# Optimization experiments

Measured on AMD Instinct MI355X. Metric: run time of the kernel, lower is better.

## Reference

```python
import jax, jax.numpy as jnp
import numpy as np

B, C, H, W = 4, 192, 56, 56


def setup_inputs() -> dict:
    key = jax.random.key(0)
    k1, k2, k3 = jax.random.split(key, 3)
    x = jax.random.normal(k1, (B, C, H, W), dtype=jnp.float32)
    conv_w = jax.random.normal(k2, (C, 2 * C), dtype=jnp.float32) * (1.0 / np.sqrt(2 * C))
    conv_b = jax.random.normal(k3, (C,), dtype=jnp.float32) * 0.01
    bn_gamma = jnp.ones((C,), dtype=jnp.float32)
    bn_beta = jnp.zeros((C,), dtype=jnp.float32)
    bn_mean = jnp.zeros((C,), dtype=jnp.float32)
    bn_var = jnp.ones((C,), dtype=jnp.float32)
    return {"x": x, "conv_w": conv_w, "conv_b": conv_b, "bn_gamma": bn_gamma,
            "bn_beta": bn_beta, "bn_mean": bn_mean, "bn_var": bn_var, "K": 4}


def reference(x, conv_w, conv_b, bn_gamma, bn_beta, bn_mean, bn_var, K):
    b, c, h, w = x.shape
    shifts_h = list(range(0, h, K))          # rolls along H
    shifts_w = list(range(K, w, K))          # rolls along W
    n = len(shifts_h) + len(shifts_w)
    scale = n ** (-0.5)
    # (B, n, C, H, W): all circularly shifted copies (static shift set)
    rolled = jnp.stack([jnp.roll(x, i, axis=2) for i in shifts_h] +
                       [jnp.roll(x, j, axis=3) for j in shifts_w], axis=1)
    # scores: tanh(scale * x * x_rolled), summed over channels -> (B, n, 1, H, W)
    scores = jnp.tanh(rolled * x[:, None] * scale).sum(axis=2, keepdims=True)
    weights = jax.nn.softmax(scores, axis=1)
    out = (rolled * weights).sum(axis=1)     # (B, C, H, W)
    cat = jnp.concatenate([x, out], axis=1)  # (B, 2C, H, W)
    # 1x1 conv as GEMM over channels
    y = jnp.einsum('bchw,oc->bohw', cat, conv_w) + conv_b[None, :, None, None]
    # BatchNorm2d in eval mode (running stats)
    eps = 1e-5
    inv = bn_gamma / jnp.sqrt(bn_var + eps)
    y = (y - bn_mean[None, :, None, None]) * inv[None, :, None, None] + bn_beta[None, :, None, None]
    return jax.nn.gelu(y, approximate=False)
```

## Files before the change

### kernel.cpp

```cpp
#include <hip/hip_runtime.h>
#include <hip/hip_bf16.h>
#include <math.h>

#define BB 4
#define CC 192
#define HH 56
#define WW 56
#define HWW 3136

typedef __attribute__((ext_vector_type(8))) short short8;
typedef __attribute__((ext_vector_type(4))) float f32x4;

__device__ __forceinline__ unsigned short f2b(float f) {
    __hip_bfloat16 h = __float2bfloat16(f);
    return __builtin_bit_cast(unsigned short, h);
}
__device__ __forceinline__ float b2f(unsigned short u) {
    unsigned int x = ((unsigned int)u) << 16;
    return __builtin_bit_cast(float, x);
}
__device__ __forceinline__ void fma4(float4& a, float w, const float4& x) {
    a.x += w * x.x; a.y += w * x.y; a.z += w * x.z; a.w += w * x.w;
}

__global__ __launch_bounds__(256) void k_pre(const float* __restrict__ x,
                                             const float* __restrict__ cw,
                                             float* __restrict__ xt,
                                             unsigned short* __restrict__ cwh,
                                             unsigned short* __restrict__ cwl) {
    int tid = threadIdx.x, bid = blockIdx.x;
    if (bid < 2352) {
        __shared__ float tile[32][33];
        int b = bid / 588, rem = bid % 588;
        int by = rem / 98, bx = rem % 98;
        int tx = tid & 31, ty = tid >> 5;
        int p0 = bx * 32, c0 = by * 32;
#pragma unroll
        for (int i = 0; i < 4; i++) {
            int c = c0 + ty + 8 * i;
            tile[ty + 8 * i][tx] = x[(b * CC + c) * HWW + p0 + tx];
        }
        __syncthreads();
#pragma unroll
        for (int i = 0; i < 4; i++) {
            int p = p0 + ty + 8 * i;
            xt[(size_t)(b * HWW + p) * CC + c0 + tx] = tile[tx][ty + 8 * i];
        }
    } else {
        int i = (bid - 2352) * 256 + tid;
        if (i < 384 * 192) {
            int n = i / 192, k = i % 192;
            float v = (n < 192) ? cw[n * 384 + k] : cw[(n - 192) * 384 + 192 + k];
            unsigned short hi = f2b(v);
            cwh[i] = hi;
            cwl[i] = f2b(v - b2f(hi));
        }
    }
}

__global__ __launch_bounds__(256) void k_mid(const float* __restrict__ xt,
                                             const unsigned short* __restrict__ cwh,
                                             const unsigned short* __restrict__ cwl,
                                             float* __restrict__ sp,
                                             float* __restrict__ u,
                                             float* __restrict__ z) {
    __shared__ __align__(16) char smem[36864];
    int tid = threadIdx.x, bid = blockIdx.x;

    if (bid < 1792) {
        float* Xs = (float*)smem;
        const float K2 = 0.38490017945975050f;
        bool isH = bid < 896;
        int lid = isH ? bid : bid - 896;
        int half = lid & 1;
        int rp = (lid >> 1) & 1;
        int cb2 = lid >> 2;
        int b = cb2 / 56, l0 = cb2 % 56;
        int r0 = rp * 2;

        const float* src = xt + (size_t)(b * HWW) * CC + half * 96;
        for (int idx = tid; idx < 28 * 24; idx += 256) {
            int t2 = idx / 24, cq = idx % 24;
            int pi = (r0 + t2 / 14) + 4 * (t2 % 14);
            int pix = isH ? (pi * WW + l0) : (l0 * WW + pi);
            float4 v = *(const float4*)(src + (size_t)pix * CC + cq * 4);
            *(float4*)&Xs[t2 * 100 + cq * 4] = v;
        }
        __syncthreads();

        int perCls = isH ? 105 : 91;
        if (tid < 2 * perCls) {
            int cls = tid / perCls, p = tid % perCls;
            int a, bb;
            if (isH) {
                a = (int)((sqrtf((float)(8 * p + 1)) - 1.0f) * 0.5f);
                bb = p - (a * (a + 1)) / 2;
            } else {
                int ap = (int)((sqrtf((float)(8 * p + 1)) - 1.0f) * 0.5f);
                bb = p - (ap * (ap + 1)) / 2;
                a = ap + 1;
            }
            const float* pA = &Xs[(cls * 14 + a) * 100];
            const float* pB = &Xs[(cls * 14 + bb) * 100];
            float s0 = 0.f, s1 = 0.f, s2 = 0.f, s3 = 0.f;
#pragma unroll
            for (int q = 0; q < 24; q++) {
                float4 av = *(const float4*)(pA + q * 4);
                float4 bv = *(const float4*)(pB + q * 4);
                s0 += __builtin_amdgcn_rcpf(__expf(av.x * bv.x * K2) + 1.0f);
                s1 += __builtin_amdgcn_rcpf(__expf(av.y * bv.y * K2) + 1.0f);
                s2 += __builtin_amdgcn_rcpf(__expf(av.z * bv.z * K2) + 1.0f);
                s3 += __builtin_amdgcn_rcpf(__expf(av.w * bv.w * K2) + 1.0f);
            }
            float s = 96.0f - 2.0f * (s0 + s1 + s2 + s3);
            int r = r0 + cls;
            size_t base = (size_t)(half * BB + b) * HWW;
            if (isH) {
                int i1 = a - bb;
                int h1 = r + 4 * a, h2 = r + 4 * bb;
                sp[(base + h1 * WW + l0) * 32 + i1] = s;
                if (a != bb) sp[(base + h2 * WW + l0) * 32 + (14 - i1)] = s;
            } else {
                int d = a - bb;
                int w1 = r + 4 * a, w2 = r + 4 * bb;
                sp[(base + l0 * WW + w1) * 32 + 14 + (d - 1)] = s;
                sp[(base + l0 * WW + w2) * 32 + 14 + (13 - d)] = s;
            }
        }
        return;
    }

    {
        unsigned short* Ah = (unsigned short*)smem;
        unsigned short* Al = Ah + 64 * 72;
        unsigned short* Bh = Ah + 2 * 64 * 72;
        unsigned short* Bl = Ah + 3 * 64 * 72;
        float* Ds = (float*)smem;
        int vb = bid - 1792;
        int bm = (vb % 196) * 64, bn = (vb / 196) * 64;
        int lane = tid & 63, wv = tid >> 6;

        f32x4 acc[4] = {{0,0,0,0},{0,0,0,0},{0,0,0,0},{0,0,0,0}};

        for (int kc = 0; kc < 3; kc++) {
#pragma unroll
            for (int r2 = 0; r2 < 2; r2++) {
                int idx = tid + r2 * 256;
                int m = idx >> 3, kq = idx & 7;
                const float* s = xt + (size_t)(bm + m) * CC + kc * 64 + kq * 8;
                float4 v0 = *(const float4*)s;
                float4 v1 = *(const float4*)(s + 4);
                float vv[8] = {v0.x, v0.y, v0.z, v0.w, v1.x, v1.y, v1.z, v1.w};
                unsigned short hi[8], lo[8];
#pragma unroll
                for (int e = 0; e < 8; e++) {
                    hi[e] = f2b(vv[e]);
                    lo[e] = f2b(vv[e] - b2f(hi[e]));
                }
                *(short8*)&Ah[m * 72 + kq * 8] = *(short8*)hi;
                *(short8*)&Al[m * 72 + kq * 8] = *(short8*)lo;
                size_t bo = (size_t)(bn + m) * 192 + kc * 64 + kq * 8;
                *(short8*)&Bh[m * 72 + kq * 8] = *(const short8*)(cwh + bo);
                *(short8*)&Bl[m * 72 + kq * 8] = *(const short8*)(cwl + bo);
            }
            __syncthreads();
            int n0 = wv * 16;
            int k8 = lane >> 4;
            int col = lane & 15;
#pragma unroll
            for (int ks = 0; ks < 64; ks += 32) {
                int koff = ks + k8 * 8;
                short8 bfh = *(const short8*)&Bh[(n0 + col) * 72 + koff];
                short8 bfl = *(const short8*)&Bl[(n0 + col) * 72 + koff];
#pragma unroll
                for (int fm = 0; fm < 4; fm++) {
                    short8 afh = *(const short8*)&Ah[(fm * 16 + col) * 72 + koff];
                    short8 afl = *(const short8*)&Al[(fm * 16 + col) * 72 + koff];
                    acc[fm] = __builtin_amdgcn_mfma_f32_16x16x32_bf16(afh, bfh, acc[fm], 0, 0, 0);
                    acc[fm] = __builtin_amdgcn_mfma_f32_16x16x32_bf16(afl, bfh, acc[fm], 0, 0, 0);
                    acc[fm] = __builtin_amdgcn_mfma_f32_16x16x32_bf16(afh, bfl, acc[fm], 0, 0, 0);
                }
            }
            __syncthreads();
        }
        {
            int col = lane & 15, rowq = lane >> 4;
#pragma unroll
            for (int fm = 0; fm < 4; fm++)
#pragma unroll
                for (int rg = 0; rg < 4; rg++)
                    Ds[(fm * 16 + rowq * 4 + rg) * 68 + wv * 16 + col] = acc[fm][rg];
        }
        __syncthreads();
        {
            int c4 = tid & 15, m0 = tid >> 4;
            int cg = bn + c4 * 4;
            float* dst = (cg < 192) ? u : z;
            int cc = (cg < 192) ? cg : cg - 192;
#pragma unroll
            for (int p = 0; p < 4; p++) {
                int m = m0 + p * 16;
                float4 v = *(float4*)&Ds[m * 68 + c4 * 4];
                *(float4*)&dst[(size_t)(bm + m) * CC + cc] = v;
            }
        }
    }
}

__global__ __launch_bounds__(192) void k_accH(const float* __restrict__ u,
                                              const float* __restrict__ z,
                                              const float* __restrict__ sp,
                                              float* __restrict__ yp) {
    __shared__ float Wt[14 * 56];
    int bid = blockIdx.x, tid = threadIdx.x;
    int b = bid / 56, l0 = bid % 56;

    if (tid < 56) {
        int pix = tid * WW + l0;
        const float4* p0 = (const float4*)&sp[((size_t)(0 * BB + b) * HWW + pix) * 32];
        const float4* p1 = (const float4*)&sp[((size_t)(1 * BB + b) * HWW + pix) * 32];
        float sc[28];
#pragma unroll
        for (int j = 0; j < 7; j++) {
            float4 a = p0[j], v = p1[j];
            sc[4 * j + 0] = a.x + v.x; sc[4 * j + 1] = a.y + v.y;
            sc[4 * j + 2] = a.z + v.z; sc[4 * j + 3] = a.w + v.w;
        }
        float mx = -1e30f;
#pragma unroll
        for (int s = 0; s < 27; s++) mx = fmaxf(mx, sc[s]);
        float sum = 0.f;
#pragma unroll
        for (int s = 0; s < 27; s++) { sc[s] = __expf(sc[s] - mx); sum += sc[s]; }
        float inv = __builtin_amdgcn_rcpf(sum);
#pragma unroll
        for (int i = 0; i < 14; i++) Wt[i * 56 + tid] = sc[i] * inv;
    }
    __syncthreads();
    {
        int r = tid & 3, q = tid >> 2;
        float4 in[14];
#pragma unroll
        for (int t = 0; t < 14; t++) {
            int pix = (r + 4 * t) * WW + l0;
            in[t] = *(const float4*)(z + (size_t)(b * HWW + pix) * CC + q * 4);
        }
        float4 acc[14];
#pragma unroll
        for (int a = 0; a < 14; a++) {
            int pix = (r + 4 * a) * WW + l0;
            acc[a] = *(const float4*)(u + (size_t)(b * HWW + pix) * CC + q * 4);
        }
#pragma unroll
        for (int i = 0; i < 14; i++)
#pragma unroll
            for (int a = 0; a < 14; a++)
                fma4(acc[a], Wt[i * 56 + (r + 4 * a)], in[(a - i + 14) % 14]);
#pragma unroll
        for (int a = 0; a < 14; a++) {
            int pix = (r + 4 * a) * WW + l0;
            *(float4*)(yp + (size_t)(b * HWW + pix) * CC + q * 4) = acc[a];
        }
    }
}

__global__ __launch_bounds__(192) void k_accW(const float* __restrict__ yp,
                                              const float* __restrict__ z,
                                              const float* __restrict__ sp,
                                              const float* __restrict__ cb,
                                              const float* __restrict__ gma,
                                              const float* __restrict__ bta,
                                              const float* __restrict__ mea,
                                              const float* __restrict__ var,
                                              float* __restrict__ y) {
    __shared__ float Wt[14 * 56];
    __shared__ float Ys[56 * 196];
    int bid = blockIdx.x, tid = threadIdx.x;
    int b = bid / 56, l0 = bid % 56;

    if (tid < 56) {
        int pix = l0 * WW + tid;
        const float4* p0 = (const float4*)&sp[((size_t)(0 * BB + b) * HWW + pix) * 32];
        const float4* p1 = (const float4*)&sp[((size_t)(1 * BB + b) * HWW + pix) * 32];
        float sc[28];
#pragma unroll
        for (int j = 0; j < 7; j++) {
            float4 a = p0[j], v = p1[j];
            sc[4 * j + 0] = a.x + v.x; sc[4 * j + 1] = a.y + v.y;
            sc[4 * j + 2] = a.z + v.z; sc[4 * j + 3] = a.w + v.w;
        }
        float mx = -1e30f;
#pragma unroll
        for (int s = 0; s < 27; s++) mx = fmaxf(mx, sc[s]);
        float sum = 0.f;
#pragma unroll
        for (int s = 0; s < 27; s++) { sc[s] = __expf(sc[s] - mx); sum += sc[s]; }
        float inv = __builtin_amdgcn_rcpf(sum);
#pragma unroll
        for (int j = 0; j < 13; j++) Wt[j * 56 + tid] = sc[14 + j] * inv;
    }
    __syncthreads();
    {
        int r = tid & 3, q = tid >> 2;
        float4 in[14];
#pragma unroll
        for (int t = 0; t < 14; t++) {
            int pix = l0 * WW + (r + 4 * t);
            in[t] = *(const float4*)(z + (size_t)(b * HWW + pix) * CC + q * 4);
        }
        float4 acc[14];
#pragma unroll
        for (int a = 0; a < 14; a++) {
            int pix = l0 * WW + (r + 4 * a);
            acc[a] = *(const float4*)(yp + (size_t)(b * HWW + pix) * CC + q * 4);
        }
#pragma unroll
        for (int j = 0; j < 13; j++)
#pragma unroll
            for (int a = 0; a < 14; a++)
                fma4(acc[a], Wt[j * 56 + (r + 4 * a)], in[(a - j - 1 + 14) % 14]);

        float4 bias4 = *(const float4*)&cb[q * 4];
        float4 g4 = *(const float4*)&gma[q * 4];
        float4 bt4 = *(const float4*)&bta[q * 4];
        float4 me4 = *(const float4*)&mea[q * 4];
        float4 va4 = *(const float4*)&var[q * 4];
        float inv0 = g4.x * rsqrtf(va4.x + 1e-5f);
        float inv1 = g4.y * rsqrtf(va4.y + 1e-5f);
        float inv2 = g4.z * rsqrtf(va4.z + 1e-5f);
        float inv3 = g4.w * rsqrtf(va4.w + 1e-5f);
#pragma unroll
        for (int a = 0; a < 14; a++) {
            int w = r + 4 * a;
            float4 t = acc[a];
            t.x = (t.x + bias4.x - me4.x) * inv0 + bt4.x;
            t.y = (t.y + bias4.y - me4.y) * inv1 + bt4.y;
            t.z = (t.z + bias4.z - me4.z) * inv2 + bt4.z;
            t.w = (t.w + bias4.w - me4.w) * inv3 + bt4.w;
            t.x = 0.5f * t.x * (1.0f + erff(t.x * 0.70710678118654752f));
            t.y = 0.5f * t.y * (1.0f + erff(t.y * 0.70710678118654752f));
            t.z = 0.5f * t.z * (1.0f + erff(t.z * 0.70710678118654752f));
            t.w = 0.5f * t.w * (1.0f + erff(t.w * 0.70710678118654752f));
            *(float4*)&Ys[w * 196 + q * 4] = t;
        }
    }
    __syncthreads();
    {
        int c = tid;
#pragma unroll
        for (int w4 = 0; w4 < 14; w4++) {
            float4 v;
            v.x = Ys[(w4 * 4 + 0) * 196 + c];
            v.y = Ys[(w4 * 4 + 1) * 196 + c];
            v.z = Ys[(w4 * 4 + 2) * 196 + c];
            v.w = Ys[(w4 * 4 + 3) * 196 + c];
            *(float4*)&y[(size_t)(b * CC + c) * HWW + l0 * WW + w4 * 4] = v;
        }
    }
}

extern "C" void kernel_launch(void* const* d_in, const int* in_sizes, int n_in,
                              void* d_out, int out_size, void* d_ws, size_t ws_size,
                              hipStream_t stream) {
    const float* x   = (const float*)d_in[0];
    const float* cw  = (const float*)d_in[1];
    const float* cb  = (const float*)d_in[2];
    const float* gma = (const float*)d_in[3];
    const float* bta = (const float*)d_in[4];
    const float* mea = (const float*)d_in[5];
    const float* var = (const float*)d_in[6];
    float* out = (float*)d_out;

    float* ws = (float*)d_ws;
    float*          xt  = ws;
    float*          sp  = ws + 2408448;
    float*          u   = ws + 3211264;
    float*          z   = ws + 5619712;
    float*          yp  = ws + 8028160;
    unsigned short* cwh = (unsigned short*)(ws + 10436608);
    unsigned short* cwl = (unsigned short*)(ws + 10473472);

    k_pre<<<2640, 256, 0, stream>>>(x, cw, xt, cwh, cwl);
    k_mid<<<2968, 256, 0, stream>>>(xt, cwh, cwl, sp, u, z);
    k_accH<<<224, 192, 0, stream>>>(u, z, sp, yp);
    k_accW<<<224, 192, 0, stream>>>(yp, z, sp, cb, gma, bta, mea, var, out);
}
```

Baseline: 127.9 us.

## Split softmax into its own kernel and fuse H/W accumulation with epilogue

Moves the per-pixel softmax over the 27 shift scores into a separate small kernel that writes normalized weights. The H-roll and W-roll accumulation passes are merged into one kernel tiled by (batch, residue r, 8-channel group, half of H). Each block stages a 14x56x8 slab of z in shared memory, so both shift directions read from LDS. This removes the yp intermediate round trip and gives 768 blocks instead of 224 for better occupancy. In exchange, each thread reloads 28 weights per pixel from global memory, and the output store writes one float per thread with a stride across channels.

```diff
diff --git a/kernel.cpp b/kernel.cpp
--- a/kernel.cpp
+++ b/kernel.cpp
@@ -18,9 +18,6 @@
 __device__ __forceinline__ float b2f(unsigned short u) {
     unsigned int x = ((unsigned int)u) << 16;
     return __builtin_bit_cast(float, x);
-}
-__device__ __forceinline__ void fma4(float4& a, float w, const float4& x) {
-    a.x += w * x.x; a.y += w * x.y; a.z += w * x.z; a.w += w * x.w;
 }
 
 __global__ __launch_bounds__(256) void k_pre(const float* __restrict__ x,
@@ -207,155 +204,117 @@
     }
 }
 
-__global__ __launch_bounds__(192) void k_accH(const float* __restrict__ u,
-                                              const float* __restrict__ z,
-                                              const float* __restrict__ sp,
-                                              float* __restrict__ yp) {
-    __shared__ float Wt[14 * 56];
-    int bid = blockIdx.x, tid = threadIdx.x;
-    int b = bid / 56, l0 = bid % 56;
-
-    if (tid < 56) {
-        int pix = tid * WW + l0;
-        const float4* p0 = (const float4*)&sp[((size_t)(0 * BB + b) * HWW + pix) * 32];
-        const float4* p1 = (const float4*)&sp[((size_t)(1 * BB + b) * HWW + pix) * 32];
-        float sc[28];
-#pragma unroll
-        for (int j = 0; j < 7; j++) {
-            float4 a = p0[j], v = p1[j];
-            sc[4 * j + 0] = a.x + v.x; sc[4 * j + 1] = a.y + v.y;
-            sc[4 * j + 2] = a.z + v.z; sc[4 * j + 3] = a.w + v.w;
-        }
-        float mx = -1e30f;
-#pragma unroll
-        for (int s = 0; s < 27; s++) mx = fmaxf(mx, sc[s]);
-        float sum = 0.f;
-#pragma unroll
-        for (int s = 0; s < 27; s++) { sc[s] = __expf(sc[s] - mx); sum += sc[s]; }
-        float inv = __builtin_amdgcn_rcpf(sum);
-#pragma unroll
-        for (int i = 0; i < 14; i++) Wt[i * 56 + tid] = sc[i] * inv;
+__global__ __launch_bounds__(256) void k_soft(const float* __restrict__ sp,
+                                              float* __restrict__ wn) {
+    int gp = blockIdx.x * 256 + threadIdx.x;
+    const float4* p0 = (const float4*)&sp[(size_t)gp * 32];
+    const float4* p1 = (const float4*)&sp[((size_t)(4 * HWW) + gp) * 32];
+    float sc[28];
+#pragma unroll
+    for (int j = 0; j < 7; j++) {
+        float4 a = p0[j], v = p1[j];
+        sc[4 * j + 0] = a.x + v.x; sc[4 * j + 1] = a.y + v.y;
+        sc[4 * j + 2] = a.z + v.z; sc[4 * j + 3] = a.w + v.w;
+    }
+    float mx = -1e30f;
+#pragma unroll
+    for (int s = 0; s < 27; s++) mx = fmaxf(mx, sc[s]);
+    float sum = 0.f;
+#pragma unroll
+    for (int s = 0; s < 27; s++) { sc[s] = __expf(sc[s] - mx); sum += sc[s]; }
+    float inv = __builtin_amdgcn_rcpf(sum);
+#pragma unroll
+    for (int s = 0; s < 27; s++) sc[s] *= inv;
+    sc[27] = 0.f;
+    float4* dst = (float4*)(wn + (size_t)gp * 28);
+#pragma unroll
+    for (int j = 0; j < 7; j++)
+        dst[j] = make_float4(sc[4 * j], sc[4 * j + 1], sc[4 * j + 2], sc[4 * j + 3]);
+}
+
+__global__ __launch_bounds__(448) void k_accHW(const float* __restrict__ u,
+                                               const float* __restrict__ z,
+                                               const float* __restrict__ wn,
+                                               const float* __restrict__ cb,
+                                               const float* __restrict__ gma,
+                                               const float* __restrict__ bta,
+                                               const float* __restrict__ mea,
+                                               const float* __restrict__ var,
+                                               float* __restrict__ y) {
+    __shared__ float Zs[14 * 56 * 8];
+    int tid = threadIdx.x, bid = blockIdx.x;
+    int th = bid & 1;
+    int t1 = bid >> 1;
+    int cc = t1 % 24;
+    int t2 = t1 / 24;
+    int r = t2 & 3;
+    int b = t2 >> 2;
+    int w = tid >> 3, c = tid & 7;
+    int cg = cc * 8 + c;
+
+#pragma unroll
+    for (int it = 0; it < 2; it++) {
+        int idx = tid + it * 448;
+        if (idx < 784) {
+            int t = idx / 56, ww = idx - t * 56;
+            const float* s = z + ((size_t)(b * HWW + (r + 4 * t) * WW + ww)) * CC + cc * 8;
+            float4 v0 = *(const float4*)s;
+            float4 v1 = *(const float4*)(s + 4);
+            float* d = &Zs[(t * 56 + ww) * 8];
+            *(float4*)d = v0;
+            *(float4*)(d + 4) = v1;
+        }
     }
     __syncthreads();
-    {
-        int r = tid & 3, q = tid >> 2;
-        float4 in[14];
-#pragma unroll
-        for (int t = 0; t < 14; t++) {
-            int pix = (r + 4 * t) * WW + l0;
-            in[t] = *(const float4*)(z + (size_t)(b * HWW + pix) * CC + q * 4);
-        }
-        float4 acc[14];
-#pragma unroll
-        for (int a = 0; a < 14; a++) {
-            int pix = (r + 4 * a) * WW + l0;
-            acc[a] = *(const float4*)(u + (size_t)(b * HWW + pix) * CC + q * 4);
-        }
+
+    float zc[14];
+#pragma unroll
+    for (int m = 0; m < 14; m++) {
+        int t0 = m + th * 7;
+        if (t0 >= 14) t0 -= 14;
+        zc[m] = Zs[(t0 * 56 + w) * 8 + c];
+    }
+
+    float bias = cb[cg];
+    float ginv = gma[cg] * rsqrtf(var[cg] + 1e-5f);
+    float bt = bta[cg];
+    float me = mea[cg];
+
+    int hbase = r + 4 * (th * 7);
+    float acc[7];
+#pragma unroll
+    for (int tt = 0; tt < 7; tt++) {
+        int pix = (hbase + 4 * tt) * WW + w;
+        acc[tt] = u[((size_t)(b * HWW + pix)) * CC + cg];
+    }
+
+#pragma unroll
+    for (int tt = 0; tt < 7; tt++) {
+        int t = th * 7 + tt;
+        int pix = (hbase + 4 * tt) * WW + w;
+        size_t gp = (size_t)b * HWW + pix;
+        const float4* wp = (const float4*)(wn + gp * 28);
+        float wt[28];
+        *(float4*)&wt[0]  = wp[0];
+        *(float4*)&wt[4]  = wp[1];
+        *(float4*)&wt[8]  = wp[2];
+        *(float4*)&wt[12] = wp[3];
+        *(float4*)&wt[16] = wp[4];
+        *(float4*)&wt[20] = wp[5];
+        *(float4*)&wt[24] = wp[6];
+        float a = acc[tt];
 #pragma unroll
         for (int i = 0; i < 14; i++)
-#pragma unroll
-            for (int a = 0; a < 14; a++)
-                fma4(acc[a], Wt[i * 56 + (r + 4 * a)], in[(a - i + 14) % 14]);
-#pragma unroll
-        for (int a = 0; a < 14; a++) {
-            int pix = (r + 4 * a) * WW + l0;
-            *(float4*)(yp + (size_t)(b * HWW + pix) * CC + q * 4) = acc[a];
-        }
-    }
-}
-
-__global__ __launch_bounds__(192) void k_accW(const float* __restrict__ yp,
-                                              const float* __restrict__ z,
-                                              const float* __restrict__ sp,
-                                              const float* __restrict__ cb,
-                                              const float* __restrict__ gma,
-                                              const float* __restrict__ bta,
-                                              const float* __restrict__ mea,
-                                              const float* __restrict__ var,
-                                              float* __restrict__ y) {
-    __shared__ float Wt[14 * 56];
-    __shared__ float Ys[56 * 196];
-    int bid = blockIdx.x, tid = threadIdx.x;
-    int b = bid / 56, l0 = bid % 56;
-
-    if (tid < 56) {
-        int pix = l0 * WW + tid;
-        const float4* p0 = (const float4*)&sp[((size_t)(0 * BB + b) * HWW + pix) * 32];
-        const float4* p1 = (const float4*)&sp[((size_t)(1 * BB + b) * HWW + pix) * 32];
-        float sc[28];
-#pragma unroll
-        for (int j = 0; j < 7; j++) {
-            float4 a = p0[j], v = p1[j];
-            sc[4 * j + 0] = a.x + v.x; sc[4 * j + 1] = a.y + v.y;
-            sc[4 * j + 2] = a.z + v.z; sc[4 * j + 3] = a.w + v.w;
-        }
-        float mx = -1e30f;
-#pragma unroll
-        for (int s = 0; s < 27; s++) mx = fmaxf(mx, sc[s]);
-        float sum = 0.f;
-#pragma unroll
-        for (int s = 0; s < 27; s++) { sc[s] = __expf(sc[s] - mx); sum += sc[s]; }
-        float inv = __builtin_amdgcn_rcpf(sum);
-#pragma unroll
-        for (int j = 0; j < 13; j++) Wt[j * 56 + tid] = sc[14 + j] * inv;
-    }
-    __syncthreads();
-    {
-        int r = tid & 3, q = tid >> 2;
-        float4 in[14];
-#pragma unroll
-        for (int t = 0; t < 14; t++) {
-            int pix = l0 * WW + (r + 4 * t);
-            in[t] = *(const float4*)(z + (size_t)(b * HWW + pix) * CC + q * 4);
-        }
-        float4 acc[14];
-#pragma unroll
-        for (int a = 0; a < 14; a++) {
-            int pix = l0 * WW + (r + 4 * a);
-            acc[a] = *(const float4*)(yp + (size_t)(b * HWW + pix) * CC + q * 4);
-        }
-#pragma unroll
-        for (int j = 0; j < 13; j++)
-#pragma unroll
-            for (int a = 0; a < 14; a++)
-                fma4(acc[a], Wt[j * 56 + (r + 4 * a)], in[(a - j - 1 + 14) % 14]);
-
-        float4 bias4 = *(const float4*)&cb[q * 4];
-        float4 g4 = *(const float4*)&gma[q * 4];
-        float4 bt4 = *(const float4*)&bta[q * 4];
-        float4 me4 = *(const float4*)&mea[q * 4];
-        float4 va4 = *(const float4*)&var[q * 4];
-        float inv0 = g4.x * rsqrtf(va4.x + 1e-5f);
-        float inv1 = g4.y * rsqrtf(va4.y + 1e-5f);
-        float inv2 = g4.z * rsqrtf(va4.z + 1e-5f);
-        float inv3 = g4.w * rsqrtf(va4.w + 1e-5f);
-#pragma unroll
-        for (int a = 0; a < 14; a++) {
-            int w = r + 4 * a;
-            float4 t = acc[a];
-            t.x = (t.x + bias4.x - me4.x) * inv0 + bt4.x;
-            t.y = (t.y + bias4.y - me4.y) * inv1 + bt4.y;
-            t.z = (t.z + bias4.z - me4.z) * inv2 + bt4.z;
-            t.w = (t.w + bias4.w - me4.w) * inv3 + bt4.w;
-            t.x = 0.5f * t.x * (1.0f + erff(t.x * 0.70710678118654752f));
-            t.y = 0.5f * t.y * (1.0f + erff(t.y * 0.70710678118654752f));
-            t.z = 0.5f * t.z * (1.0f + erff(t.z * 0.70710678118654752f));
-            t.w = 0.5f * t.w * (1.0f + erff(t.w * 0.70710678118654752f));
-            *(float4*)&Ys[w * 196 + q * 4] = t;
-        }
-    }
-    __syncthreads();
-    {
-        int c = tid;
-#pragma unroll
-        for (int w4 = 0; w4 < 14; w4++) {
-            float4 v;
-            v.x = Ys[(w4 * 4 + 0) * 196 + c];
-            v.y = Ys[(w4 * 4 + 1) * 196 + c];
-            v.z = Ys[(w4 * 4 + 2) * 196 + c];
-            v.w = Ys[(w4 * 4 + 3) * 196 + c];
-            *(float4*)&y[(size_t)(b * CC + c) * HWW + l0 * WW + w4 * 4] = v;
-        }
+            a += wt[i] * zc[(tt - i + 14) % 14];
+#pragma unroll
+        for (int j = 1; j <= 13; j++) {
+            int wj = w - 4 * j;
+            if (wj < 0) wj += 56;
+            a += wt[13 + j] * Zs[(t * 56 + wj) * 8 + c];
+        }
+        float v = (a + bias - me) * ginv + bt;
+        v = 0.5f * v * (1.0f + erff(v * 0.70710678118654752f));
+        y[((size_t)(b * CC + cg)) * HWW + pix] = v;
     }
 }
 
@@ -376,12 +335,12 @@
     float*          sp  = ws + 2408448;
     float*          u   = ws + 3211264;
     float*          z   = ws + 5619712;
-    float*          yp  = ws + 8028160;
+    float*          wn  = ws + 8028160;
     unsigned short* cwh = (unsigned short*)(ws + 10436608);
     unsigned short* cwl = (unsigned short*)(ws + 10473472);
 
     k_pre<<<2640, 256, 0, stream>>>(x, cw, xt, cwh, cwl);
     k_mid<<<2968, 256, 0, stream>>>(xt, cwh, cwl, sp, u, z);
-    k_accH<<<224, 192, 0, stream>>>(u, z, sp, yp);
-    k_accW<<<224, 192, 0, stream>>>(yp, z, sp, cb, gma, bta, mea, var, out);
-}
+    k_soft<<<49, 256, 0, stream>>>(sp, wn);
+    k_accHW<<<768, 448, 0, stream>>>(u, z, wn, cb, gma, bta, mea, var, out);
+}
```

After: 131.6 us. 1.03x slower.
